# Performance work log

Measured on AMD Instinct MI355X. Metric: run time of the kernel, lower is better.

## Reference

```python
import jax, jax.numpy as jnp
import numpy as np

B, S, HID, H = 4, 2048, 1024, 16
D = HID // H  # dim per head


def setup_inputs() -> dict:
    key = jax.random.key(0)
    ks = jax.random.split(key, 7)
    inp = {
        "q": jax.random.normal(ks[0], (B, S, HID), dtype=jnp.float32),
        "k": jax.random.normal(ks[1], (B, S, HID), dtype=jnp.float32),
        "v": jax.random.normal(ks[2], (B, S, HID), dtype=jnp.float32),
        # Linear weights stored as (in, out); applied as x @ W. use_bias=False.
        "Wq": jax.random.normal(ks[3], (HID, HID), dtype=jnp.float32) * (1.0 / np.sqrt(HID)),
        "Wk": jax.random.normal(ks[4], (HID, HID), dtype=jnp.float32) * (1.0 / np.sqrt(HID)),
        "Wv": jax.random.normal(ks[5], (HID, HID), dtype=jnp.float32) * (1.0 / np.sqrt(HID)),
        "Wo": jax.random.normal(ks[6], (HID, HID), dtype=jnp.float32) * (1.0 / np.sqrt(HID)),
    }
    return inp


def reference(q, k, v, Wq, Wk, Wv, Wo):
    scale = 1.0 / jnp.sqrt(jnp.float32(D))
    # QKV projections, then split hidden into (H, D) heads (same layout as transpose_qkv)
    Q = (q @ Wq).reshape(B, S, H, D)
    K = (k @ Wk).reshape(B, S, H, D)
    V = (v @ Wv).reshape(B, S, H, D)
    # scaled dot-product attention: full [B,H,S,S] score matrix, softmax over keys
    attn_w = jnp.einsum("bqhd,bkhd->bhqk", Q, K) * scale
    attn_w = jax.nn.softmax(attn_w, axis=-1)
    # dropout rate is 0 (eval-mode / deterministic)
    O = jnp.einsum("bhqk,bkhd->bqhd", attn_w, V).reshape(B, S, HID)
    return O @ Wo
```

## Files before the change

kernel.cpp:

```cpp
#include <hip/hip_runtime.h>


typedef __attribute__((ext_vector_type(8))) short short8;
typedef __attribute__((ext_vector_type(4))) float float4v;

#if __has_builtin(__builtin_amdgcn_exp2f)
#define EXP2F(x) __builtin_amdgcn_exp2f(x)
#else
#define EXP2F(x) exp2f(x)
#endif

__device__ __forceinline__ unsigned short f2b(float x) {
  unsigned u = __float_as_uint(x);
  u = (u + 0x7fffu + ((u >> 16) & 1u)) >> 16;
  return (unsigned short)u;
}
__device__ __forceinline__ unsigned int pk2(float a, float b) {
  return (unsigned)f2b(a) | ((unsigned)f2b(b) << 16);
}

typedef __attribute__((address_space(3))) unsigned int lds_uint;
typedef const __attribute__((address_space(1))) unsigned int gbl_uint;
__device__ __forceinline__ void stage16(const unsigned short* g, unsigned short* l) {
#if __has_builtin(__builtin_amdgcn_global_load_lds)
  __builtin_amdgcn_global_load_lds((gbl_uint*)g, (lds_uint*)l, 16, 0, 0);
#else
  *(uint4*)l = *(const uint4*)g;
#endif
}

__global__ __launch_bounds__(256) void conv_qkv(const float* __restrict__ q,
                                                const float* __restrict__ k,
                                                const float* __restrict__ v,
                                                unsigned short* __restrict__ ws,
                                                float qscale) {
  const int z = blockIdx.y;
  const float* src = z == 0 ? q : (z == 1 ? k : v);
  unsigned short* dst = ws + (size_t)z * 8388608;
  const float s = z == 0 ? qscale : 1.0f;
  size_t i = ((size_t)blockIdx.x * 256 + threadIdx.x) * 8;
  float4v a = *(const float4v*)(src + i);
  float4v b = *(const float4v*)(src + i + 4);
  uint4 o;
  o.x = pk2(a.x * s, a.y * s);
  o.y = pk2(a.z * s, a.w * s);
  o.z = pk2(b.x * s, b.y * s);
  o.w = pk2(b.z * s, b.w * s);
  *(uint4*)(dst + i) = o;
}

__global__ __launch_bounds__(256) void wtrans(const float* __restrict__ Wq,
                                              const float* __restrict__ Wk,
                                              const float* __restrict__ Wv,
                                              const float* __restrict__ Wo,
                                              unsigned short* __restrict__ Wt) {
  __shared__ float tile[32][33];
  const float* W = blockIdx.z == 0 ? Wq : blockIdx.z == 1 ? Wk
                   : blockIdx.z == 2 ? Wv : Wo;
  unsigned short* T = Wt + (size_t)blockIdx.z * 1048576;
  const int tx = threadIdx.x & 31, ty = threadIdx.x >> 5;
  const int k0 = blockIdx.y * 32, n0 = blockIdx.x * 32;
#pragma unroll
  for (int i = 0; i < 4; i++)
    tile[ty + 8 * i][tx] = W[(size_t)(k0 + ty + 8 * i) * 1024 + n0 + tx];
  __syncthreads();
#pragma unroll
  for (int i = 0; i < 4; i++)
    T[(size_t)(n0 + ty + 8 * i) * 1024 + k0 + tx] = f2b(tile[tx][ty + 8 * i]);
}

template <int MODE>
__global__ __launch_bounds__(256, 2) void gemm_bt(const unsigned short* __restrict__ A,
                                                  const unsigned short* __restrict__ Bt,
                                                  void* __restrict__ Cg) {
  __shared__ __align__(16) unsigned short As[128 * 64];
  __shared__ __align__(16) unsigned short Bs[128 * 64];
  const int tid = threadIdx.x;
  const int lane = tid & 63;
  const int w = tid >> 6;
  const int quad = lane >> 4, col = lane & 15;
  const int wm = w >> 1, wn = w & 1;
  const int m0 = blockIdx.y * 128;
  const int n0 = blockIdx.x * 128;
  const int rA = lane >> 3, cA = lane & 7;

  float4v acc[4][4] = {};

  for (int k0 = 0; k0 < 1024; k0 += 64) {
    __syncthreads();
#pragma unroll
    for (int j = 0; j < 4; j++) {
      const int row = w * 32 + j * 8 + rA;
      stage16(A + (size_t)(m0 + row) * 1024 + k0 + ((cA ^ rA) * 8),
              &As[row * 64 + cA * 8]);
      stage16(Bt + (size_t)(n0 + row) * 1024 + k0 + ((cA ^ rA) * 8),
              &Bs[row * 64 + cA * 8]);
    }
    __syncthreads();

#pragma unroll
    for (int ks = 0; ks < 2; ks++) {
      short8 af[4], bf[4];
#pragma unroll
      for (int mi = 0; mi < 4; mi++) {
        int row = wm * 64 + mi * 16 + col;
        af[mi] = *(const short8*)&As[row * 64 + (((ks * 4 + quad) ^ (col & 7)) * 8)];
      }
#pragma unroll
      for (int ni = 0; ni < 4; ni++) {
        int row = wn * 64 + ni * 16 + col;
        bf[ni] = *(const short8*)&Bs[row * 64 + (((ks * 4 + quad) ^ (col & 7)) * 8)];
      }
#pragma unroll
      for (int mi = 0; mi < 4; mi++)
#pragma unroll
        for (int ni = 0; ni < 4; ni++)
          acc[mi][ni] = __builtin_amdgcn_mfma_f32_16x16x32_bf16(af[mi], bf[ni],
                                                                acc[mi][ni], 0, 0, 0);
    }
  }

#pragma unroll
  for (int mi = 0; mi < 4; mi++) {
#pragma unroll
    for (int ni = 0; ni < 4; ni++) {
#pragma unroll
      for (int r = 0; r < 4; r++) {
        int row = m0 + wm * 64 + mi * 16 + quad * 4 + r;
        int cg = n0 + wn * 64 + ni * 16 + col;
        float v = acc[mi][ni][r];
        if (MODE == 0) {
          ((unsigned short*)Cg)[((((row >> 11) << 4) + (cg >> 6)) * 2048 +
                                 (row & 2047)) * 64 + (cg & 63)] = f2b(v);
        } else if (MODE == 1) {
          ((unsigned short*)Cg)[(((((row >> 11) << 4) + (cg >> 6)) << 6) +
                                 (cg & 63)) * 2048 + (row & 2047)] = f2b(v);
        } else {
          ((float*)Cg)[(size_t)row * 1024 + cg] = v;
        }
      }
    }
  }
}

__global__ __launch_bounds__(256, 2) void attn_kernel(
    const unsigned short* __restrict__ Qb, const unsigned short* __restrict__ Kb,
    const unsigned short* __restrict__ Vt, unsigned short* __restrict__ Ob) {
  __shared__ __align__(16) unsigned short K_lds[128 * 64];
  __shared__ __align__(16) unsigned short V_lds[64 * 128];
  __shared__ __align__(16) unsigned short P_lds[128 * 128];
  __shared__ float den_lds[128];

  const int tid = threadIdx.x;
  const int lane = tid & 63;
  const int w = tid >> 6;
  const int quad = lane >> 4, col = lane & 15;
  const int wq = w >> 1, wk = w & 1;
  const int bh = blockIdx.y;
  const int qt = blockIdx.x;

  const unsigned short* Kbase = Kb + (size_t)bh * (2048 * 64);
  const unsigned short* Vbase = Vt + (size_t)bh * (64 * 2048);

  short8 qf[4][2];
#pragma unroll
  for (int mi = 0; mi < 4; mi++)
#pragma unroll
    for (int ks = 0; ks < 2; ks++) {
      int s = qt * 128 + wq * 64 + mi * 16 + col;
      qf[mi][ks] = *(const short8*)(Qb + ((size_t)bh * 2048 + s) * 64 + ks * 32 + quad * 8);
    }

  float4v oacc[4][2] = {};
  float dens[4][4] = {};

  const int rK = lane >> 3, cK = lane & 7;
  const int rV = lane >> 4, cV = lane & 15;

  for (int kt = 0; kt < 16; kt++) {
    const int s0 = kt * 128;
    __syncthreads();
#pragma unroll
    for (int j = 0; j < 4; j++) {
      const int rowK = w * 32 + j * 8 + rK;
      stage16(Kbase + (size_t)(s0 + rowK) * 64 + ((cK ^ rK) * 8),
              &K_lds[rowK * 64 + cK * 8]);
      const int rowV = w * 16 + j * 4 + rV;
      stage16(Vbase + (size_t)rowV * 2048 + s0 + (((cV ^ (rowV & 15)) & 15) * 8),
              &V_lds[rowV * 128 + cV * 8]);
    }
    __syncthreads();

    float4v sacc[4][4] = {};
    short8 kf[4][2];
#pragma unroll
    for (int ni = 0; ni < 4; ni++)
#pragma unroll
      for (int ks = 0; ks < 2; ks++) {
        int row = wk * 64 + ni * 16 + col;
        kf[ni][ks] = *(const short8*)&K_lds[row * 64 +
                                            (((ks * 4 + quad) ^ (col & 7)) * 8)];
      }
#pragma unroll
    for (int mi = 0; mi < 4; mi++)
#pragma unroll
      for (int ni = 0; ni < 4; ni++)
#pragma unroll
        for (int ks = 0; ks < 2; ks++)
          sacc[mi][ni] = __builtin_amdgcn_mfma_f32_16x16x32_bf16(
              qf[mi][ks], kf[ni][ks], sacc[mi][ni], 0, 0, 0);

#pragma unroll
    for (int mi = 0; mi < 4; mi++) {
      const int qb_ = wq * 64 + mi * 16 + quad * 4;
#pragma unroll
      for (int ni = 0; ni < 4; ni++) {
        const int c0 = wk * 8 + ni * 2;
#pragma unroll
        for (int r = 0; r < 4; r++) {
          float p = EXP2F(sacc[mi][ni][r]);
          dens[mi][r] += p;
          const int q = qb_ + r;
          P_lds[q * 128 + (((c0 + (col >> 3)) ^ (quad * 4 + r)) * 8) + (col & 7)] =
              f2b(p);
        }
      }
    }
    __syncthreads();

#pragma unroll
    for (int ks = 0; ks < 4; ks++) {
      short8 pf[4], vf[2];
#pragma unroll
      for (int mi = 0; mi < 4; mi++) {
        int row = wq * 64 + mi * 16 + col;
        pf[mi] = *(const short8*)&P_lds[row * 128 + ((((ks * 4 + quad) ^ col) & 15) * 8)];
      }
#pragma unroll
      for (int nv = 0; nv < 2; nv++) {
        int row = wk * 32 + nv * 16 + col;
        vf[nv] = *(const short8*)&V_lds[row * 128 + ((((ks * 4 + quad) ^ col) & 15) * 8)];
      }
#pragma unroll
      for (int mi = 0; mi < 4; mi++)
#pragma unroll
        for (int nv = 0; nv < 2; nv++)
          oacc[mi][nv] = __builtin_amdgcn_mfma_f32_16x16x32_bf16(
              pf[mi], vf[nv], oacc[mi][nv], 0, 0, 0);
    }
  }

  if (tid < 128) den_lds[tid] = 0.f;
  __syncthreads();
#pragma unroll
  for (int mi = 0; mi < 4; mi++)
#pragma unroll
    for (int r = 0; r < 4; r++) {
      float v = dens[mi][r];
      v += __shfl_xor(v, 1);
      v += __shfl_xor(v, 2);
      v += __shfl_xor(v, 4);
      v += __shfl_xor(v, 8);
      if (col == 0) atomicAdd(&den_lds[wq * 64 + mi * 16 + quad * 4 + r], v);
    }
  __syncthreads();

  const int b = bh >> 4, h = bh & 15;
#pragma unroll
  for (int mi = 0; mi < 4; mi++) {
#pragma unroll
    for (int r = 0; r < 4; r++) {
      int srow = qt * 128 + wq * 64 + mi * 16 + quad * 4 + r;
      float rd = 1.f / den_lds[wq * 64 + mi * 16 + quad * 4 + r];
#pragma unroll
      for (int nv = 0; nv < 2; nv++) {
        int dc = wk * 32 + nv * 16 + col;
        Ob[((size_t)b * 2048 + srow) * 1024 + h * 64 + dc] = f2b(oacc[mi][nv][r] * rd);
      }
    }
  }
}

extern "C" void kernel_launch(void* const* d_in, const int* in_sizes, int n_in,
                              void* d_out, int out_size, void* d_ws, size_t ws_size,
                              hipStream_t stream) {
  const float* q = (const float*)d_in[0];
  const float* k = (const float*)d_in[1];
  const float* v = (const float*)d_in[2];
  const float* Wq = (const float*)d_in[3];
  const float* Wk = (const float*)d_in[4];
  const float* Wv = (const float*)d_in[5];
  const float* Wo = (const float*)d_in[6];

  unsigned short* ws = (unsigned short*)d_ws;
  unsigned short* qb = ws;
  unsigned short* kb = ws + 8388608;
  unsigned short* vb = ws + 16777216;
  unsigned short* Qb = ws + 25165824;
  unsigned short* Kb = ws + 33554432;
  unsigned short* Vt = ws + 41943040;
  unsigned short* Wt = ws + 50331648;

  dim3 blk(256);
  const float qscale = 0.18033688011112042f;

  conv_qkv<<<dim3(4096, 3), blk, 0, stream>>>(q, k, v, ws, qscale);
  wtrans<<<dim3(32, 32, 4), blk, 0, stream>>>(Wq, Wk, Wv, Wo, Wt);

  dim3 gp(8, 64);
  gemm_bt<0><<<gp, blk, 0, stream>>>(qb, Wt + 0 * 1048576, Qb);
  gemm_bt<0><<<gp, blk, 0, stream>>>(kb, Wt + 1 * 1048576, Kb);
  gemm_bt<1><<<gp, blk, 0, stream>>>(vb, Wt + 2 * 1048576, Vt);

  attn_kernel<<<dim3(16, 64), blk, 0, stream>>>(Qb, Kb, Vt, qb );

  gemm_bt<2><<<gp, blk, 0, stream>>>(qb , Wt + 3 * 1048576, (float*)d_out);
}
```

Measured before the change: 357.2 us.

## Swap MFMA operands to vectorize epilogue stores and simplify bf16 packing

```diff
diff --git a/kernel.cpp b/kernel.cpp
--- a/kernel.cpp
+++ b/kernel.cpp
@@ -11,12 +11,12 @@
 #endif
 
 __device__ __forceinline__ unsigned short f2b(float x) {
-  unsigned u = __float_as_uint(x);
-  u = (u + 0x7fffu + ((u >> 16) & 1u)) >> 16;
-  return (unsigned short)u;
-}
-__device__ __forceinline__ unsigned int pk2(float a, float b) {
-  return (unsigned)f2b(a) | ((unsigned)f2b(b) << 16);
+  return (unsigned short)((__float_as_uint(x) + 0x8000u) >> 16);
+}
+__device__ __forceinline__ unsigned pk2f(float a, float b) {
+  unsigned ua = __float_as_uint(a) + 0x8000u;
+  unsigned ub = __float_as_uint(b) + 0x8000u;
+  return __builtin_amdgcn_perm(ub, ua, 0x07060302);
 }
 
 typedef __attribute__((address_space(3))) unsigned int lds_uint;
@@ -42,10 +42,10 @@
   float4v a = *(const float4v*)(src + i);
   float4v b = *(const float4v*)(src + i + 4);
   uint4 o;
-  o.x = pk2(a.x * s, a.y * s);
-  o.y = pk2(a.z * s, a.w * s);
-  o.z = pk2(b.x * s, b.y * s);
-  o.w = pk2(b.z * s, b.w * s);
+  o.x = pk2f(a.x * s, a.y * s);
+  o.y = pk2f(a.z * s, a.w * s);
+  o.z = pk2f(b.x * s, b.y * s);
+  o.w = pk2f(b.z * s, b.w * s);
   *(uint4*)(dst + i) = o;
 }
 
@@ -69,7 +69,7 @@
     T[(size_t)(n0 + ty + 8 * i) * 1024 + k0 + tx] = f2b(tile[tx][ty + 8 * i]);
 }
 
-template <int MODE>
+template <int MODE, bool SWAP>
 __global__ __launch_bounds__(256, 2) void gemm_bt(const unsigned short* __restrict__ A,
                                                   const unsigned short* __restrict__ Bt,
                                                   void* __restrict__ Cg) {
@@ -91,9 +91,9 @@
 #pragma unroll
     for (int j = 0; j < 4; j++) {
       const int row = w * 32 + j * 8 + rA;
-      stage16(A + (size_t)(m0 + row) * 1024 + k0 + ((cA ^ rA) * 8),
+      stage16(A + (unsigned)(m0 + row) * 1024 + k0 + ((cA ^ rA) * 8),
               &As[row * 64 + cA * 8]);
-      stage16(Bt + (size_t)(n0 + row) * 1024 + k0 + ((cA ^ rA) * 8),
+      stage16(Bt + (unsigned)(n0 + row) * 1024 + k0 + ((cA ^ rA) * 8),
               &Bs[row * 64 + cA * 8]);
     }
     __syncthreads();
@@ -114,30 +114,59 @@
 #pragma unroll
       for (int mi = 0; mi < 4; mi++)
 #pragma unroll
-        for (int ni = 0; ni < 4; ni++)
-          acc[mi][ni] = __builtin_amdgcn_mfma_f32_16x16x32_bf16(af[mi], bf[ni],
-                                                                acc[mi][ni], 0, 0, 0);
-    }
-  }
-
-#pragma unroll
-  for (int mi = 0; mi < 4; mi++) {
+        for (int ni = 0; ni < 4; ni++) {
+          if (SWAP)
+            acc[ni][mi] = __builtin_amdgcn_mfma_f32_16x16x32_bf16(
+                bf[ni], af[mi], acc[ni][mi], 0, 0, 0);
+          else
+            acc[mi][ni] = __builtin_amdgcn_mfma_f32_16x16x32_bf16(
+                af[mi], bf[ni], acc[mi][ni], 0, 0, 0);
+        }
+    }
+  }
+
+  if (MODE == 0) {
 #pragma unroll
     for (int ni = 0; ni < 4; ni++) {
-#pragma unroll
-      for (int r = 0; r < 4; r++) {
-        int row = m0 + wm * 64 + mi * 16 + quad * 4 + r;
-        int cg = n0 + wn * 64 + ni * 16 + col;
-        float v = acc[mi][ni][r];
-        if (MODE == 0) {
-          ((unsigned short*)Cg)[((((row >> 11) << 4) + (cg >> 6)) * 2048 +
-                                 (row & 2047)) * 64 + (cg & 63)] = f2b(v);
-        } else if (MODE == 1) {
-          ((unsigned short*)Cg)[(((((row >> 11) << 4) + (cg >> 6)) << 6) +
-                                 (cg & 63)) * 2048 + (row & 2047)] = f2b(v);
-        } else {
-          ((float*)Cg)[(size_t)row * 1024 + cg] = v;
-        }
+      const int cg = n0 + wn * 64 + ni * 16 + quad * 4;
+      const int h = cg >> 6, dlo = cg & 63;
+#pragma unroll
+      for (int mi = 0; mi < 4; mi++) {
+        const int tok = m0 + wm * 64 + mi * 16 + col;
+        const int b = tok >> 11, s = tok & 2047;
+        uint2 pk;
+        pk.x = pk2f(acc[ni][mi][0], acc[ni][mi][1]);
+        pk.y = pk2f(acc[ni][mi][2], acc[ni][mi][3]);
+        *(uint2*)((unsigned short*)Cg +
+                  ((unsigned)((b * 16 + h) * 2048 + s) * 64 + dlo)) = pk;
+      }
+    }
+  } else if (MODE == 1) {
+#pragma unroll
+    for (int mi = 0; mi < 4; mi++) {
+      const int tok = m0 + wm * 64 + mi * 16 + quad * 4;
+      const int b = tok >> 11, s = tok & 2047;
+#pragma unroll
+      for (int ni = 0; ni < 4; ni++) {
+        const int cg = n0 + wn * 64 + ni * 16 + col;
+        const int h = cg >> 6, d = cg & 63;
+        uint2 pk;
+        pk.x = pk2f(acc[mi][ni][0], acc[mi][ni][1]);
+        pk.y = pk2f(acc[mi][ni][2], acc[mi][ni][3]);
+        *(uint2*)((unsigned short*)Cg +
+                  ((unsigned)((b * 16 + h) * 64 + d) * 2048 + s)) = pk;
+      }
+    }
+  } else {
+#pragma unroll
+    for (int mi = 0; mi < 4; mi++) {
+      const int row = m0 + wm * 64 + mi * 16 + quad * 4;
+#pragma unroll
+      for (int ni = 0; ni < 4; ni++) {
+        const int cg = n0 + wn * 64 + ni * 16 + col;
+#pragma unroll
+        for (int r = 0; r < 4; r++)
+          ((float*)Cg)[(unsigned)(row + r) * 1024 + cg] = acc[mi][ni][r];
       }
     }
   }
@@ -164,15 +193,17 @@
 
   short8 qf[4][2];
 #pragma unroll
-  for (int mi = 0; mi < 4; mi++)
+  for (int qi = 0; qi < 4; qi++)
 #pragma unroll
     for (int ks = 0; ks < 2; ks++) {
-      int s = qt * 128 + wq * 64 + mi * 16 + col;
-      qf[mi][ks] = *(const short8*)(Qb + ((size_t)bh * 2048 + s) * 64 + ks * 32 + quad * 8);
-    }
-
-  float4v oacc[4][2] = {};
-  float dens[4][4] = {};
+      int s = qt * 128 + wq * 64 + qi * 16 + col;
+      qf[qi][ks] = *(const short8*)(Qb + ((size_t)bh * 2048 + s) * 64 + ks * 32 + quad * 8);
+    }
+
+  float4v oacc[2][4] = {};
+  float dens[4] = {};
+
+  if (tid < 128) den_lds[tid] = 0.f;
 
   const int rK = lane >> 3, cK = lane & 7;
   const int rV = lane >> 4, cV = lane & 15;
@@ -183,10 +214,10 @@
 #pragma unroll
     for (int j = 0; j < 4; j++) {
       const int rowK = w * 32 + j * 8 + rK;
-      stage16(Kbase + (size_t)(s0 + rowK) * 64 + ((cK ^ rK) * 8),
+      stage16(Kbase + (unsigned)(s0 + rowK) * 64 + ((cK ^ rK) * 8),
               &K_lds[rowK * 64 + cK * 8]);
       const int rowV = w * 16 + j * 4 + rV;
-      stage16(Vbase + (size_t)rowV * 2048 + s0 + (((cV ^ (rowV & 15)) & 15) * 8),
+      stage16(Vbase + (unsigned)rowV * 2048 + s0 + (((cV ^ (rowV & 15)) & 15) * 8),
               &V_lds[rowV * 128 + cV * 8]);
     }
     __syncthreads();
@@ -194,36 +225,38 @@
     float4v sacc[4][4] = {};
     short8 kf[4][2];
 #pragma unroll
-    for (int ni = 0; ni < 4; ni++)
+    for (int ki = 0; ki < 4; ki++)
 #pragma unroll
       for (int ks = 0; ks < 2; ks++) {
-        int row = wk * 64 + ni * 16 + col;
-        kf[ni][ks] = *(const short8*)&K_lds[row * 64 +
+        int row = wk * 64 + ki * 16 + col;
+        kf[ki][ks] = *(const short8*)&K_lds[row * 64 +
                                             (((ks * 4 + quad) ^ (col & 7)) * 8)];
       }
 #pragma unroll
-    for (int mi = 0; mi < 4; mi++)
-#pragma unroll
-      for (int ni = 0; ni < 4; ni++)
+    for (int ki = 0; ki < 4; ki++)
+#pragma unroll
+      for (int qi = 0; qi < 4; qi++)
 #pragma unroll
         for (int ks = 0; ks < 2; ks++)
-          sacc[mi][ni] = __builtin_amdgcn_mfma_f32_16x16x32_bf16(
-              qf[mi][ks], kf[ni][ks], sacc[mi][ni], 0, 0, 0);
-
-#pragma unroll
-    for (int mi = 0; mi < 4; mi++) {
-      const int qb_ = wq * 64 + mi * 16 + quad * 4;
-#pragma unroll
-      for (int ni = 0; ni < 4; ni++) {
-        const int c0 = wk * 8 + ni * 2;
-#pragma unroll
-        for (int r = 0; r < 4; r++) {
-          float p = EXP2F(sacc[mi][ni][r]);
-          dens[mi][r] += p;
-          const int q = qb_ + r;
-          P_lds[q * 128 + (((c0 + (col >> 3)) ^ (quad * 4 + r)) * 8) + (col & 7)] =
-              f2b(p);
-        }
+          sacc[ki][qi] = __builtin_amdgcn_mfma_f32_16x16x32_bf16(
+              kf[ki][ks], qf[qi][ks], sacc[ki][qi], 0, 0, 0);
+
+#pragma unroll
+    for (int ki = 0; ki < 4; ki++) {
+      const int c = wk * 8 + ki * 2 + (quad >> 1);
+      const int hh = quad & 1;
+#pragma unroll
+      for (int qi = 0; qi < 4; qi++) {
+        const int q = wq * 64 + qi * 16 + col;
+        float p0 = EXP2F(sacc[ki][qi][0]);
+        float p1 = EXP2F(sacc[ki][qi][1]);
+        float p2 = EXP2F(sacc[ki][qi][2]);
+        float p3 = EXP2F(sacc[ki][qi][3]);
+        dens[qi] += (p0 + p1) + (p2 + p3);
+        uint2 pk;
+        pk.x = pk2f(p0, p1);
+        pk.y = pk2f(p2, p3);
+        *(uint2*)&P_lds[q * 128 + ((c ^ col) & 15) * 8 + hh * 4] = pk;
       }
     }
     __syncthreads();
@@ -242,41 +275,36 @@
         vf[nv] = *(const short8*)&V_lds[row * 128 + ((((ks * 4 + quad) ^ col) & 15) * 8)];
       }
 #pragma unroll
-      for (int mi = 0; mi < 4; mi++)
-#pragma unroll
-        for (int nv = 0; nv < 2; nv++)
-          oacc[mi][nv] = __builtin_amdgcn_mfma_f32_16x16x32_bf16(
-              pf[mi], vf[nv], oacc[mi][nv], 0, 0, 0);
-    }
-  }
-
-  if (tid < 128) den_lds[tid] = 0.f;
+      for (int nv = 0; nv < 2; nv++)
+#pragma unroll
+        for (int mi = 0; mi < 4; mi++)
+          oacc[nv][mi] = __builtin_amdgcn_mfma_f32_16x16x32_bf16(
+              vf[nv], pf[mi], oacc[nv][mi], 0, 0, 0);
+    }
+  }
+
+#pragma unroll
+  for (int qi = 0; qi < 4; qi++) {
+    float v = dens[qi];
+    v += __shfl_xor(v, 16);
+    v += __shfl_xor(v, 32);
+    if (lane < 16) atomicAdd(&den_lds[wq * 64 + qi * 16 + col], v);
+  }
   __syncthreads();
-#pragma unroll
-  for (int mi = 0; mi < 4; mi++)
-#pragma unroll
-    for (int r = 0; r < 4; r++) {
-      float v = dens[mi][r];
-      v += __shfl_xor(v, 1);
-      v += __shfl_xor(v, 2);
-      v += __shfl_xor(v, 4);
-      v += __shfl_xor(v, 8);
-      if (col == 0) atomicAdd(&den_lds[wq * 64 + mi * 16 + quad * 4 + r], v);
-    }
-  __syncthreads();
 
   const int b = bh >> 4, h = bh & 15;
 #pragma unroll
   for (int mi = 0; mi < 4; mi++) {
-#pragma unroll
-    for (int r = 0; r < 4; r++) {
-      int srow = qt * 128 + wq * 64 + mi * 16 + quad * 4 + r;
-      float rd = 1.f / den_lds[wq * 64 + mi * 16 + quad * 4 + r];
-#pragma unroll
-      for (int nv = 0; nv < 2; nv++) {
-        int dc = wk * 32 + nv * 16 + col;
-        Ob[((size_t)b * 2048 + srow) * 1024 + h * 64 + dc] = f2b(oacc[mi][nv][r] * rd);
-      }
+    const int srow = qt * 128 + wq * 64 + mi * 16 + col;
+    const float rd = 1.f / den_lds[wq * 64 + mi * 16 + col];
+    unsigned base = (unsigned)(b * 2048 + srow) * 1024 + h * 64;
+#pragma unroll
+    for (int nv = 0; nv < 2; nv++) {
+      const int d0 = wk * 32 + nv * 16 + quad * 4;
+      uint2 pk;
+      pk.x = pk2f(oacc[nv][mi][0] * rd, oacc[nv][mi][1] * rd);
+      pk.y = pk2f(oacc[nv][mi][2] * rd, oacc[nv][mi][3] * rd);
+      *(uint2*)(Ob + base + d0) = pk;
     }
   }
 }
@@ -308,11 +336,11 @@
   wtrans<<<dim3(32, 32, 4), blk, 0, stream>>>(Wq, Wk, Wv, Wo, Wt);
 
   dim3 gp(8, 64);
-  gemm_bt<0><<<gp, blk, 0, stream>>>(qb, Wt + 0 * 1048576, Qb);
-  gemm_bt<0><<<gp, blk, 0, stream>>>(kb, Wt + 1 * 1048576, Kb);
-  gemm_bt<1><<<gp, blk, 0, stream>>>(vb, Wt + 2 * 1048576, Vt);
+  gemm_bt<0, true><<<gp, blk, 0, stream>>>(qb, Wt + 0 * 1048576, Qb);
+  gemm_bt<0, true><<<gp, blk, 0, stream>>>(kb, Wt + 1 * 1048576, Kb);
+  gemm_bt<1, false><<<gp, blk, 0, stream>>>(vb, Wt + 2 * 1048576, Vt);
 
   attn_kernel<<<dim3(16, 64), blk, 0, stream>>>(Qb, Kb, Vt, qb );
 
-  gemm_bt<2><<<gp, blk, 0, stream>>>(qb , Wt + 3 * 1048576, (float*)d_out);
-}
+  gemm_bt<2, false><<<gp, blk, 0, stream>>>(qb , Wt + 3 * 1048576, (float*)d_out);
+}
```

New measurement: 356.2 us. Within noise of the previous version (-0.3%).
